# Optimization experiments

Hardware: AMD Instinct MI355X
Metric: run time of the kernel (lower is better)

## Reference

```python
import jax, jax.numpy as jnp
import numpy as np

N, C, K = 8192, 512, 64


def setup_inputs() -> dict:
    key = jax.random.key(0)
    k1, k2, k3 = jax.random.split(key, 3)
    return {
        "f_i": jax.random.normal(k1, (N, C), dtype=jnp.float32),
        "f_j": jax.random.normal(k2, (N, C), dtype=jnp.float32),
        "means": jax.random.normal(k3, (K, C), dtype=jnp.float32),
        "scales": jnp.ones((K, C), dtype=jnp.float32),
        "weights": jnp.ones((K,), dtype=jnp.float32),
    }


def _neg_sq_dist(f, means, scales):
    # f: [N, C], means/scales: [K, C] -> [N, K]
    d = (f[:, None, :] - means[None, :, :]) / scales[None, :, :]
    return -jnp.sum(d * d, axis=-1)


def reference(f_i, f_j, means, scales, weights):
    # Original: kernel[n,m,k] = exp(dist_i[n,k] + dist_j[m,k]); out = kernel @ weights.
    # This factors exactly as (exp(dist_i) * w) @ exp(dist_j)^T, avoiding the
    # O(N*N*K) intermediate while computing identical math.
    dist_i = _neg_sq_dist(f_i, means, scales)  # [N, K]
    dist_j = _neg_sq_dist(f_j, means, scales)  # [N, K]
    phi_i = jnp.exp(dist_i) * weights[None, :]  # [N, K]
    phi_j = jnp.exp(dist_j)                      # [N, K]
    return phi_i @ phi_j.T                       # [N, N]
```

## Files before the change

kernel.cpp:

```cpp
#include <hip/hip_runtime.h>
#include <hip/hip_bf16.h>
#include <math.h>

#define NP   8192
#define CD   512
#define KD   64
#define TWON 16384
#define CC   1024

typedef __attribute__((ext_vector_type(8))) short short8;
typedef __attribute__((ext_vector_type(4))) float f32x4;

__device__ __forceinline__ void split_bf16(float x, __hip_bfloat16& h, __hip_bfloat16& l) {
    h = __float2bfloat16(x);
    l = __float2bfloat16(x - __bfloat162float(h));
}

__global__ __launch_bounds__(256) void prep_kernel(
    const float* __restrict__ means, const float* __restrict__ scales,
    __hip_bfloat16* __restrict__ VTT_hi, __hip_bfloat16* __restrict__ VTT_lo,
    float* __restrict__ cst)
{
    const int k = blockIdx.x;
    const int t = threadIdx.x;
    __shared__ float red[256];
    float local = 0.f;
    for (int c = t; c < CD; c += 256) {
        float m    = means[k * CD + c];
        float s    = scales[k * CD + c];
        float inv  = 1.0f / s;
        float inv2 = inv * inv;
        __hip_bfloat16 h, l;
        split_bf16(2.0f * m * inv2, h, l);
        VTT_hi[(size_t)k * CC + c] = h;
        VTT_lo[(size_t)k * CC + c] = l;
        split_bf16(-inv2, h, l);
        VTT_hi[(size_t)k * CC + CD + c] = h;
        VTT_lo[(size_t)k * CC + CD + c] = l;
        local += m * m * inv2;
    }
    red[t] = local;
    __syncthreads();
    for (int off = 128; off > 0; off >>= 1) {
        if (t < off) red[t] += red[t + off];
        __syncthreads();
    }
    if (t == 0) cst[k] = red[0];
}

__global__ __launch_bounds__(256) void phi_kernel(
    const float* __restrict__ f_i, const float* __restrict__ f_j,
    const __hip_bfloat16* __restrict__ VTT_hi,
    const __hip_bfloat16* __restrict__ VTT_lo,
    const float* __restrict__ cst, const float* __restrict__ weights,
    __hip_bfloat16* __restrict__ phi)
{
    const int t = threadIdx.x, lane = t & 63, wave = t >> 6;
    const int q = lane >> 4, m = lane & 15;
    const int base = blockIdx.x * 64 + wave * 16;
    const bool iside = (base < NP);
    const float* frow = iside ? &f_i[(size_t)(base + m) * CD]
                              : &f_j[(size_t)(base + m - NP) * CD];
    const short* BH = (const short*)VTT_hi;
    const short* BL = (const short*)VTT_lo;

    f32x4 acc[4];
    #pragma unroll
    for (int nt = 0; nt < 4; ++nt) acc[nt] = (f32x4){0.f, 0.f, 0.f, 0.f};

    for (int ch = 0; ch < 16; ++ch) {
        const int c0 = ch * 32 + q * 8;
        float4 x0 = *(const float4*)&frow[c0];
        float4 x1 = *(const float4*)&frow[c0 + 4];
        float xs[8] = {x0.x, x0.y, x0.z, x0.w, x1.x, x1.y, x1.z, x1.w};
        union { short8 v; __hip_bfloat16 h[8]; } aLh, aLl, aSh, aSl;
        #pragma unroll
        for (int j = 0; j < 8; ++j) {
            __hip_bfloat16 h, l;
            split_bf16(xs[j], h, l);          aLh.h[j] = h; aLl.h[j] = l;
            split_bf16(xs[j] * xs[j], h, l);  aSh.h[j] = h; aSl.h[j] = l;
        }
        #pragma unroll
        for (int nt = 0; nt < 4; ++nt) {
            const size_t boff = (size_t)(nt * 16 + m) * CC + c0;
            short8 bh0 = *(const short8*)&BH[boff];
            short8 bl0 = *(const short8*)&BL[boff];
            short8 bh1 = *(const short8*)&BH[boff + CD];
            short8 bl1 = *(const short8*)&BL[boff + CD];
            acc[nt] = __builtin_amdgcn_mfma_f32_16x16x32_bf16(aLh.v, bh0, acc[nt], 0, 0, 0);
            acc[nt] = __builtin_amdgcn_mfma_f32_16x16x32_bf16(aLh.v, bl0, acc[nt], 0, 0, 0);
            acc[nt] = __builtin_amdgcn_mfma_f32_16x16x32_bf16(aLl.v, bh0, acc[nt], 0, 0, 0);
            acc[nt] = __builtin_amdgcn_mfma_f32_16x16x32_bf16(aSh.v, bh1, acc[nt], 0, 0, 0);
            acc[nt] = __builtin_amdgcn_mfma_f32_16x16x32_bf16(aSh.v, bl1, acc[nt], 0, 0, 0);
            acc[nt] = __builtin_amdgcn_mfma_f32_16x16x32_bf16(aSl.v, bh1, acc[nt], 0, 0, 0);
        }
    }

    #pragma unroll
    for (int nt = 0; nt < 4; ++nt) {
        const int kout = nt * 16 + m;
        const float cs = cst[kout];
        const float wv = iside ? weights[kout] : 1.0f;
        #pragma unroll
        for (int r = 0; r < 4; ++r) {
            const int row = base + q * 4 + r;
            float ph = expf(acc[nt][r] - cs) * wv;
            phi[(size_t)row * KD + kout] = __float2bfloat16(ph);
        }
    }
}

__global__ __launch_bounds__(256) void gemm_kernel(
    const __hip_bfloat16* __restrict__ phi, float* __restrict__ out)
{
    const int t = threadIdx.x, lane = t & 63, wave = t >> 6;
    const int q = lane >> 4, m = lane & 15;
    const int i0 = blockIdx.y * 128 + (wave & 1) * 64;
    const int j0 = blockIdx.x * 128 + (wave >> 1) * 64;
    const short* phiS = (const short*)phi;

    short8 Aj[4][2], Bi[4][2];
    #pragma unroll
    for (int tt = 0; tt < 4; ++tt)
        #pragma unroll
        for (int kh = 0; kh < 2; ++kh) {
            Aj[tt][kh] = *(const short8*)
                &phiS[(size_t)(NP + j0 + tt * 16 + m) * KD + kh * 32 + q * 8];
            Bi[tt][kh] = *(const short8*)
                &phiS[(size_t)(i0 + tt * 16 + m) * KD + kh * 32 + q * 8];
        }

    f32x4 acc[4][4];
    #pragma unroll
    for (int bt = 0; bt < 4; ++bt)
        #pragma unroll
        for (int at = 0; at < 4; ++at)
            acc[bt][at] = (f32x4){0.f, 0.f, 0.f, 0.f};

    #pragma unroll
    for (int bt = 0; bt < 4; ++bt)
        #pragma unroll
        for (int at = 0; at < 4; ++at) {
            acc[bt][at] = __builtin_amdgcn_mfma_f32_16x16x32_bf16(
                Aj[at][0], Bi[bt][0], acc[bt][at], 0, 0, 0);
            acc[bt][at] = __builtin_amdgcn_mfma_f32_16x16x32_bf16(
                Aj[at][1], Bi[bt][1], acc[bt][at], 0, 0, 0);
        }

    #pragma unroll
    for (int bt = 0; bt < 4; ++bt) {
        const size_t row = (size_t)(i0 + bt * 16 + m);
        #pragma unroll
        for (int at = 0; at < 4; ++at)
            *(float4*)&out[row * NP + j0 + at * 16 + q * 4] =
                (float4){acc[bt][at][0], acc[bt][at][1],
                         acc[bt][at][2], acc[bt][at][3]};
    }
}

extern "C" void kernel_launch(void* const* d_in, const int* in_sizes, int n_in,
                              void* d_out, int out_size, void* d_ws, size_t ws_size,
                              hipStream_t stream) {
    const float* f_i     = (const float*)d_in[0];
    const float* f_j     = (const float*)d_in[1];
    const float* means   = (const float*)d_in[2];
    const float* scales  = (const float*)d_in[3];
    const float* weights = (const float*)d_in[4];
    float* out = (float*)d_out;

    char* ws = (char*)d_ws;
    __hip_bfloat16* VTT_hi = (__hip_bfloat16*)(ws);
    __hip_bfloat16* VTT_lo = (__hip_bfloat16*)(ws + 131072);
    float*          cst    = (float*)(ws + 262144);
    __hip_bfloat16* phi    = (__hip_bfloat16*)(ws + 262400);

    prep_kernel<<<64, 256, 0, stream>>>(means, scales, VTT_hi, VTT_lo, cst);
    phi_kernel<<<256, 256, 0, stream>>>(f_i, f_j, VTT_hi, VTT_lo, cst, weights, phi);
    gemm_kernel<<<dim3(64, 64), 256, 0, stream>>>(phi, out);
}
```

Baseline: 336.0 us.

## Split phi kernel over K tiles for more blocks; use nontemporal output stores

The phi kernel now launches four times as many blocks, each computing one 16-wide tile of the 64 K outputs instead of all four. This raises parallelism from 256 blocks to 1024, better filling the GPU, at the cost of each block re-reading and re-splitting the same f rows into bf16 hi/lo parts four times. Separately, the GEMM kernel writes its 256 MB fp32 output with nontemporal stores to avoid cache pollution.

New measurement: 350.9 us. 4.4% more time.

```diff
diff --git a/kernel.cpp b/kernel.cpp
--- a/kernel.cpp
+++ b/kernel.cpp
@@ -57,16 +57,15 @@
 {
     const int t = threadIdx.x, lane = t & 63, wave = t >> 6;
     const int q = lane >> 4, m = lane & 15;
-    const int base = blockIdx.x * 64 + wave * 16;
+    const int base = (blockIdx.x >> 2) * 64 + wave * 16;
+    const int kt   = (blockIdx.x & 3) * 16;
     const bool iside = (base < NP);
     const float* frow = iside ? &f_i[(size_t)(base + m) * CD]
                               : &f_j[(size_t)(base + m - NP) * CD];
     const short* BH = (const short*)VTT_hi;
     const short* BL = (const short*)VTT_lo;
 
-    f32x4 acc[4];
-    #pragma unroll
-    for (int nt = 0; nt < 4; ++nt) acc[nt] = (f32x4){0.f, 0.f, 0.f, 0.f};
+    f32x4 acc = (f32x4){0.f, 0.f, 0.f, 0.f};
 
     for (int ch = 0; ch < 16; ++ch) {
         const int c0 = ch * 32 + q * 8;
@@ -80,33 +79,27 @@
             split_bf16(xs[j], h, l);          aLh.h[j] = h; aLl.h[j] = l;
             split_bf16(xs[j] * xs[j], h, l);  aSh.h[j] = h; aSl.h[j] = l;
         }
-        #pragma unroll
-        for (int nt = 0; nt < 4; ++nt) {
-            const size_t boff = (size_t)(nt * 16 + m) * CC + c0;
-            short8 bh0 = *(const short8*)&BH[boff];
-            short8 bl0 = *(const short8*)&BL[boff];
-            short8 bh1 = *(const short8*)&BH[boff + CD];
-            short8 bl1 = *(const short8*)&BL[boff + CD];
-            acc[nt] = __builtin_amdgcn_mfma_f32_16x16x32_bf16(aLh.v, bh0, acc[nt], 0, 0, 0);
-            acc[nt] = __builtin_amdgcn_mfma_f32_16x16x32_bf16(aLh.v, bl0, acc[nt], 0, 0, 0);
-            acc[nt] = __builtin_amdgcn_mfma_f32_16x16x32_bf16(aLl.v, bh0, acc[nt], 0, 0, 0);
-            acc[nt] = __builtin_amdgcn_mfma_f32_16x16x32_bf16(aSh.v, bh1, acc[nt], 0, 0, 0);
-            acc[nt] = __builtin_amdgcn_mfma_f32_16x16x32_bf16(aSh.v, bl1, acc[nt], 0, 0, 0);
-            acc[nt] = __builtin_amdgcn_mfma_f32_16x16x32_bf16(aSl.v, bh1, acc[nt], 0, 0, 0);
-        }
+        const size_t boff = (size_t)(kt + m) * CC + c0;
+        short8 bh0 = *(const short8*)&BH[boff];
+        short8 bl0 = *(const short8*)&BL[boff];
+        short8 bh1 = *(const short8*)&BH[boff + CD];
+        short8 bl1 = *(const short8*)&BL[boff + CD];
+        acc = __builtin_amdgcn_mfma_f32_16x16x32_bf16(aLh.v, bh0, acc, 0, 0, 0);
+        acc = __builtin_amdgcn_mfma_f32_16x16x32_bf16(aLh.v, bl0, acc, 0, 0, 0);
+        acc = __builtin_amdgcn_mfma_f32_16x16x32_bf16(aLl.v, bh0, acc, 0, 0, 0);
+        acc = __builtin_amdgcn_mfma_f32_16x16x32_bf16(aSh.v, bh1, acc, 0, 0, 0);
+        acc = __builtin_amdgcn_mfma_f32_16x16x32_bf16(aSh.v, bl1, acc, 0, 0, 0);
+        acc = __builtin_amdgcn_mfma_f32_16x16x32_bf16(aSl.v, bh1, acc, 0, 0, 0);
     }
 
+    const int kout = kt + m;
+    const float cs = cst[kout];
+    const float wv = iside ? weights[kout] : 1.0f;
     #pragma unroll
-    for (int nt = 0; nt < 4; ++nt) {
-        const int kout = nt * 16 + m;
-        const float cs = cst[kout];
-        const float wv = iside ? weights[kout] : 1.0f;
-        #pragma unroll
-        for (int r = 0; r < 4; ++r) {
-            const int row = base + q * 4 + r;
-            float ph = expf(acc[nt][r] - cs) * wv;
-            phi[(size_t)row * KD + kout] = __float2bfloat16(ph);
-        }
+    for (int r = 0; r < 4; ++r) {
+        const int row = base + q * 4 + r;
+        float ph = expf(acc[r] - cs) * wv;
+        phi[(size_t)row * KD + kout] = __float2bfloat16(ph);
     }
 }
 
@@ -151,10 +144,10 @@
     for (int bt = 0; bt < 4; ++bt) {
         const size_t row = (size_t)(i0 + bt * 16 + m);
         #pragma unroll
-        for (int at = 0; at < 4; ++at)
-            *(float4*)&out[row * NP + j0 + at * 16 + q * 4] =
-                (float4){acc[bt][at][0], acc[bt][at][1],
-                         acc[bt][at][2], acc[bt][at][3]};
+        for (int at = 0; at < 4; ++at) {
+            f32x4* dst = (f32x4*)&out[row * NP + j0 + at * 16 + q * 4];
+            __builtin_nontemporal_store(acc[bt][at], dst);
+        }
     }
 }
 
@@ -175,6 +168,6 @@
     __hip_bfloat16* phi    = (__hip_bfloat16*)(ws + 262400);
 
     prep_kernel<<<64, 256, 0, stream>>>(means, scales, VTT_hi, VTT_lo, cst);
-    phi_kernel<<<256, 256, 0, stream>>>(f_i, f_j, VTT_hi, VTT_lo, cst, weights, phi);
+    phi_kernel<<<1024, 256, 0, stream>>>(f_i, f_j, VTT_hi, VTT_lo, cst, weights, phi);
     gemm_kernel<<<dim3(64, 64), 256, 0, stream>>>(phi, out);
 }
```
